# Optimization experiments

Measured on AMD Instinct MI355X. Metric: run time of the kernel, lower is better.

## Reference

```python
import jax, jax.numpy as jnp
import numpy as np

N_HEAD = 8
D = 512
D_K = D // N_HEAD  # 64
B, S = 8, 1024


def setup_inputs() -> dict:
    key = jax.random.key(0)
    ks = jax.random.split(key, 7)
    scale = 1.0 / np.sqrt(D)  # ~ torch Linear init range
    return {
        "q": jax.random.normal(ks[0], (B, S, D), dtype=jnp.float32),
        "k": jax.random.normal(ks[1], (B, S, D), dtype=jnp.float32),
        "v": jax.random.normal(ks[2], (B, S, D), dtype=jnp.float32),
        # per-head Q/K projection weights, torch Linear convention W:[out,in]=[d_k,d]
        "Wq": jax.random.uniform(ks[3], (N_HEAD, D_K, D), jnp.float32, -scale, scale),
        "Wk": jax.random.uniform(ks[4], (N_HEAD, D_K, D), jnp.float32, -scale, scale),
        "Wv": jax.random.uniform(ks[5], (D_K, D), jnp.float32, -scale, scale),
        "Wo": jax.random.uniform(ks[6], (D, D_K), jnpp := jnp.float32, -1.0 / np.sqrt(D_K), 1.0 / np.sqrt(D_K)),
    }


def reference(q, k, v, Wq, Wk, Wv, Wo):
    # shared V projection: [B,S,d_k]
    vs = jnp.einsum("bsd,ed->bse", v, Wv)
    # batched per-head Q/K projections: [B,H,S,d_k]
    qh = jnp.einsum("bsd,hed->bhse", q, Wq)
    kh = jnp.einsum("bsd,hed->bhse", k, Wk)
    inv_sqrt_dk = 1.0 / jnp.sqrt(jnp.asarray(D_K, q.dtype))
    # scores [B,H,Sq,Sk], softmax over keys
    scores = jnp.einsum("bhqe,bhke->bhqk", qh * inv_sqrt_dk, kh)
    attn = jax.nn.softmax(scores, axis=-1)
    # shared V across heads, then mean over heads (interpretable combine)
    heads = jnp.einsum("bhqk,bke->bhqe", attn, vs)  # [B,H,S,d_k]
    head = heads.mean(axis=1)                        # [B,S,d_k]
    out = jnp.einsum("bse,de->bsd", head, Wo)        # [B,S,d]
    # torch.stack(attention) stacks over heads first -> [H,B,Sq,Sk]
    attn_stacked = jnp.transpose(attn, (1, 0, 2, 3))
    return out, attn_stacked
```

## Files before the change

### kernel.cpp

```cpp
#include <hip/hip_runtime.h>


using short8 = __attribute__((ext_vector_type(8))) short;
using f32x4  = __attribute__((ext_vector_type(4))) float;

static __device__ __forceinline__ short f2bf(float f) {
    union { float f; unsigned u; } x; x.f = f;
    unsigned r = x.u + 0x7fffu + ((x.u >> 16) & 1u);
    return (short)(r >> 16);
}
static __device__ __forceinline__ float bfhi2f(unsigned hi_bits) {
    union { unsigned u; float f; } x; x.u = hi_bits;
    return x.f;
}

__global__ __launch_bounds__(256) void gemm_proj(
    const float* __restrict__ A, const float* __restrict__ W,
    void* __restrict__ out, int M, int N, int K, float scale, int mode)
{
    __shared__ short As[128][40];
    __shared__ short Bs[128][40];

    const int tid  = threadIdx.x;
    const int m0   = blockIdx.x * 128;
    const int n0   = blockIdx.y * 128;
    const int lane = tid & 63, wave = tid >> 6;
    const int wm   = (wave & 1) * 64, wn = (wave >> 1) * 64;
    const int lrow = lane & 15, lq = lane >> 4;

    f32x4 acc[4][4] = {};

    for (int k0 = 0; k0 < K; k0 += 32) {
#pragma unroll
        for (int i = 0; i < 4; ++i) {
            int c = tid + i * 256;
            int row = c >> 3, c4 = c & 7;
            float4 v = *(const float4*)(A + (size_t)(m0 + row) * K + k0 + c4 * 4);
            short* dst = &As[row][c4 * 4];
            dst[0] = f2bf(v.x); dst[1] = f2bf(v.y); dst[2] = f2bf(v.z); dst[3] = f2bf(v.w);
        }
#pragma unroll
        for (int i = 0; i < 4; ++i) {
            int c = tid + i * 256;
            int row = c >> 3, c4 = c & 7;
            int gn = n0 + row;
            float4 v = make_float4(0.f, 0.f, 0.f, 0.f);
            if (gn < N) v = *(const float4*)(W + (size_t)gn * K + k0 + c4 * 4);
            short* dst = &Bs[row][c4 * 4];
            dst[0] = f2bf(v.x); dst[1] = f2bf(v.y); dst[2] = f2bf(v.z); dst[3] = f2bf(v.w);
        }
        __syncthreads();

        short8 af[4], bw[4];
#pragma unroll
        for (int i = 0; i < 4; ++i)
            af[i] = *(const short8*)&As[wm + i * 16 + lrow][lq * 8];
#pragma unroll
        for (int j = 0; j < 4; ++j)
            bw[j] = *(const short8*)&Bs[wn + j * 16 + lrow][lq * 8];
#pragma unroll
        for (int i = 0; i < 4; ++i)
#pragma unroll
            for (int j = 0; j < 4; ++j)
                acc[i][j] = __builtin_amdgcn_mfma_f32_16x16x32_bf16(af[i], bw[j], acc[i][j], 0, 0, 0);
        __syncthreads();
    }

#pragma unroll
    for (int i = 0; i < 4; ++i) {
#pragma unroll
        for (int j = 0; j < 4; ++j) {
#pragma unroll
            for (int r = 0; r < 4; ++r) {
                int m = m0 + wm + i * 16 + lq * 4 + r;
                int n = n0 + wn + j * 16 + lrow;
                if (n >= N) continue;
                float val = acc[i][j][r] * scale;
                if (mode == 0) {
                    int b = m >> 10, s = m & 1023;
                    int hh = n >> 6, e = n & 63;
                    ((short*)out)[(((size_t)(b * 8 + hh) * 1024 + s) << 6) + e] = f2bf(val);
                } else if (mode == 2) {
                    int b = m >> 10, s = m & 1023;
                    ((short*)out)[(((size_t)b * 64 + n) << 10) + s] = f2bf(val);
                } else {
                    ((float*)out)[(size_t)m * N + n] = val;
                }
            }
        }
    }
}

__global__ __launch_bounds__(256) void attn_fused(
    const short* __restrict__ qh,
    const short* __restrict__ kh,
    const short* __restrict__ vt,
    float* __restrict__ attn_out,
    float* __restrict__ head)
{
    __shared__ short qs[64][72];
    __shared__ short ks[128][72];
    __shared__ short vts[64][136];
    __shared__ short pa[4][16][136];

    const int bh = blockIdx.x;
    const int b = bh >> 3, h = bh & 7;
    const int qbase = blockIdx.y << 6;
    const int tid  = threadIdx.x;
    const int lane = tid & 63, wave = tid >> 6;
    const int lrow = lane & 15, lq = lane >> 4;

    const short* qp = qh + ((size_t)bh << 16);
    const short* kp = kh + ((size_t)bh << 16);
    const short* vp = vt + ((size_t)b << 16);

#pragma unroll
    for (int i = 0; i < 2; ++i) {
        int c = tid + i * 256;
        int row = c >> 3, c8 = c & 7;
        *(uint4*)&qs[row][c8 * 8] = *(const uint4*)(qp + (size_t)(qbase + row) * 64 + c8 * 8);
    }
    __syncthreads();

    short8 qf[2];
#pragma unroll
    for (int kk = 0; kk < 2; ++kk)
        qf[kk] = *(const short8*)&qs[wave * 16 + lrow][kk * 32 + lq * 8];

    float sume[4] = {0.f, 0.f, 0.f, 0.f};
    for (int kt = 0; kt < 1024; kt += 128) {
        __syncthreads();
#pragma unroll
        for (int i = 0; i < 4; ++i) {
            int c = tid + i * 256;
            int row = c >> 3, c8 = c & 7;
            *(uint4*)&ks[row][c8 * 8] = *(const uint4*)(kp + (size_t)(kt + row) * 64 + c8 * 8);
        }
        __syncthreads();
#pragma unroll
        for (int j = 0; j < 8; ++j) {
            f32x4 sc = {0.f, 0.f, 0.f, 0.f};
            short8 kb0 = *(const short8*)&ks[j * 16 + lrow][lq * 8];
            short8 kb1 = *(const short8*)&ks[j * 16 + lrow][32 + lq * 8];
            sc = __builtin_amdgcn_mfma_f32_16x16x32_bf16(qf[0], kb0, sc, 0, 0, 0);
            sc = __builtin_amdgcn_mfma_f32_16x16x32_bf16(qf[1], kb1, sc, 0, 0, 0);
#pragma unroll
            for (int r = 0; r < 4; ++r) sume[r] += __expf(sc[r]);
        }
    }
#pragma unroll
    for (int m = 1; m <= 8; m <<= 1)
#pragma unroll
        for (int r = 0; r < 4; ++r) sume[r] += __shfl_xor(sume[r], m, 64);
    float rinv[4];
#pragma unroll
    for (int r = 0; r < 4; ++r) rinv[r] = 1.0f / sume[r];

    f32x4 hacc[4] = {};
    for (int kt = 0; kt < 1024; kt += 128) {
        __syncthreads();
#pragma unroll
        for (int i = 0; i < 4; ++i) {
            int c = tid + i * 256;
            int row = c >> 3, c8 = c & 7;
            *(uint4*)&ks[row][c8 * 8] = *(const uint4*)(kp + (size_t)(kt + row) * 64 + c8 * 8);
        }
#pragma unroll
        for (int i = 0; i < 4; ++i) {
            int c = tid + i * 256;
            int row = c >> 4, c8 = c & 15;
            *(uint4*)&vts[row][c8 * 8] = *(const uint4*)(vp + ((size_t)row << 10) + kt + c8 * 8);
        }
        __syncthreads();

#pragma unroll
        for (int j = 0; j < 8; ++j) {
            f32x4 sc = {0.f, 0.f, 0.f, 0.f};
            short8 kb0 = *(const short8*)&ks[j * 16 + lrow][lq * 8];
            short8 kb1 = *(const short8*)&ks[j * 16 + lrow][32 + lq * 8];
            sc = __builtin_amdgcn_mfma_f32_16x16x32_bf16(qf[0], kb0, sc, 0, 0, 0);
            sc = __builtin_amdgcn_mfma_f32_16x16x32_bf16(qf[1], kb1, sc, 0, 0, 0);
#pragma unroll
            for (int r = 0; r < 4; ++r)
                pa[wave][lq * 4 + r][j * 16 + lrow] = f2bf(__expf(sc[r]) * rinv[r]);
        }

        size_t abase = (((size_t)(h * 8 + b) * 1024 + qbase + wave * 16) << 10) + kt;
#pragma unroll
        for (int i = 0; i < 4; ++i) {
            int c = lane + i * 64;
            int row = c >> 4, c8 = c & 15;
            uint4 pk = *(const uint4*)&pa[wave][row][c8 * 8];
            float4 v0, v1;
            v0.x = bfhi2f(pk.x << 16); v0.y = bfhi2f(pk.x & 0xffff0000u);
            v0.z = bfhi2f(pk.y << 16); v0.w = bfhi2f(pk.y & 0xffff0000u);
            v1.x = bfhi2f(pk.z << 16); v1.y = bfhi2f(pk.z & 0xffff0000u);
            v1.z = bfhi2f(pk.w << 16); v1.w = bfhi2f(pk.w & 0xffff0000u);
            float* gdst = attn_out + abase + ((size_t)row << 10) + c8 * 8;
            *(float4*)gdst       = v0;
            *(float4*)(gdst + 4) = v1;
        }

#pragma unroll
        for (int kk = 0; kk < 4; ++kk) {
            short8 af = *(const short8*)&pa[wave][lrow][kk * 32 + lq * 8];
#pragma unroll
            for (int cc = 0; cc < 4; ++cc) {
                short8 bv = *(const short8*)&vts[cc * 16 + lrow][kk * 32 + lq * 8];
                hacc[cc] = __builtin_amdgcn_mfma_f32_16x16x32_bf16(af, bv, hacc[cc], 0, 0, 0);
            }
        }
    }

#pragma unroll
    for (int cc = 0; cc < 4; ++cc)
#pragma unroll
        for (int r = 0; r < 4; ++r) {
            float v = hacc[cc][r] * 0.125f;
            atomicAdd(&head[(((size_t)b * 1024 + qbase + wave * 16 + lq * 4 + r) << 6) + cc * 16 + lrow], v);
        }
}

extern "C" void kernel_launch(void* const* d_in, const int* in_sizes, int n_in,
                              void* d_out, int out_size, void* d_ws, size_t ws_size,
                              hipStream_t stream)
{
    (void)in_sizes; (void)n_in; (void)out_size; (void)ws_size;

    const float* q  = (const float*)d_in[0];
    const float* k  = (const float*)d_in[1];
    const float* v  = (const float*)d_in[2];
    const float* Wq = (const float*)d_in[3];
    const float* Wk = (const float*)d_in[4];
    const float* Wv = (const float*)d_in[5];
    const float* Wo = (const float*)d_in[6];

    float* out  = (float*)d_out;
    float* attn = out + (size_t)8 * 1024 * 512;

    char* ws = (char*)d_ws;
    short* qh  = (short*)(ws);
    short* kh  = (short*)(ws + ((size_t)8  << 20));
    short* vt  = (short*)(ws + ((size_t)16 << 20));
    float* head = (float*)(ws + ((size_t)17 << 20));

    hipMemsetAsync(head, 0, (size_t)8 * 1024 * 64 * sizeof(float), stream);

    gemm_proj<<<dim3(64, 4), 256, 0, stream>>>(q, Wq, qh, 8192, 512, 512, 0.125f, 0);
    gemm_proj<<<dim3(64, 4), 256, 0, stream>>>(k, Wk, kh, 8192, 512, 512, 1.0f, 0);
    gemm_proj<<<dim3(64, 1), 256, 0, stream>>>(v, Wv, vt, 8192, 64, 512, 1.0f, 2);

    attn_fused<<<dim3(64, 16), 256, 0, stream>>>(qh, kh, vt, attn, head);

    gemm_proj<<<dim3(64, 4), 256, 0, stream>>>(head, Wo, out, 8192, 512, 64, 1.0f, 3);
}
```

Before: 517.4 us.

## Merge projection launches, widen attention blocks, use nontemporal attn stores

The three Q/K/V projection GEMMs become one launch that picks its operands from blockIdx.y, and the output GEMM gets its own specialised kernel. The attention kernel now runs 512 threads covering 128 query rows per block, so each K/V tile loaded into LDS is shared by twice as many waves, halving K/V reloads. Attention probability stores use nontemporal writes to avoid polluting caches with the large write-once output. The larger blocks use more LDS and mean fewer blocks overall, which may lower occupancy.

```diff
diff --git a/kernel.cpp b/kernel.cpp
--- a/kernel.cpp
+++ b/kernel.cpp
@@ -14,16 +14,25 @@
     return x.f;
 }
 
-__global__ __launch_bounds__(256) void gemm_proj(
-    const float* __restrict__ A, const float* __restrict__ W,
-    void* __restrict__ out, int M, int N, int K, float scale, int mode)
+__global__ __launch_bounds__(256) void proj_all(
+    const float* __restrict__ q, const float* __restrict__ k,
+    const float* __restrict__ v,
+    const float* __restrict__ Wq, const float* __restrict__ Wk,
+    const float* __restrict__ Wv,
+    short* __restrict__ qh, short* __restrict__ kh, short* __restrict__ vt)
 {
     __shared__ short As[128][40];
     __shared__ short Bs[128][40];
 
+    const int y = blockIdx.y;
+    const float* A; const float* W; short* out; int N; float scale; int mode; int n0;
+    if (y < 4)      { A = q; W = Wq; out = qh; N = 512; scale = 0.125f; mode = 0; n0 = y << 7; }
+    else if (y < 8) { A = k; W = Wk; out = kh; N = 512; scale = 1.0f;   mode = 0; n0 = (y - 4) << 7; }
+    else            { A = v; W = Wv; out = vt; N = 64;  scale = 1.0f;   mode = 2; n0 = 0; }
+
+    const int K = 512;
     const int tid  = threadIdx.x;
     const int m0   = blockIdx.x * 128;
-    const int n0   = blockIdx.y * 128;
     const int lane = tid & 63, wave = tid >> 6;
     const int wm   = (wave & 1) * 64, wn = (wave >> 1) * 64;
     const int lrow = lane & 15, lq = lane >> 4;
@@ -35,19 +44,19 @@
         for (int i = 0; i < 4; ++i) {
             int c = tid + i * 256;
             int row = c >> 3, c4 = c & 7;
-            float4 v = *(const float4*)(A + (size_t)(m0 + row) * K + k0 + c4 * 4);
+            float4 vv = *(const float4*)(A + (size_t)(m0 + row) * K + k0 + c4 * 4);
             short* dst = &As[row][c4 * 4];
-            dst[0] = f2bf(v.x); dst[1] = f2bf(v.y); dst[2] = f2bf(v.z); dst[3] = f2bf(v.w);
+            dst[0] = f2bf(vv.x); dst[1] = f2bf(vv.y); dst[2] = f2bf(vv.z); dst[3] = f2bf(vv.w);
         }
 #pragma unroll
         for (int i = 0; i < 4; ++i) {
             int c = tid + i * 256;
             int row = c >> 3, c4 = c & 7;
             int gn = n0 + row;
-            float4 v = make_float4(0.f, 0.f, 0.f, 0.f);
-            if (gn < N) v = *(const float4*)(W + (size_t)gn * K + k0 + c4 * 4);
+            float4 vv = make_float4(0.f, 0.f, 0.f, 0.f);
+            if (gn < N) vv = *(const float4*)(W + (size_t)gn * K + k0 + c4 * 4);
             short* dst = &Bs[row][c4 * 4];
-            dst[0] = f2bf(v.x); dst[1] = f2bf(v.y); dst[2] = f2bf(v.z); dst[3] = f2bf(v.w);
+            dst[0] = f2bf(vv.x); dst[1] = f2bf(vv.y); dst[2] = f2bf(vv.z); dst[3] = f2bf(vv.w);
         }
         __syncthreads();
 
@@ -79,33 +88,96 @@
                 if (mode == 0) {
                     int b = m >> 10, s = m & 1023;
                     int hh = n >> 6, e = n & 63;
-                    ((short*)out)[(((size_t)(b * 8 + hh) * 1024 + s) << 6) + e] = f2bf(val);
-                } else if (mode == 2) {
+                    out[(((size_t)(b * 8 + hh) * 1024 + s) << 6) + e] = f2bf(val);
+                } else {
                     int b = m >> 10, s = m & 1023;
-                    ((short*)out)[(((size_t)b * 64 + n) << 10) + s] = f2bf(val);
-                } else {
-                    ((float*)out)[(size_t)m * N + n] = val;
+                    out[(((size_t)b * 64 + n) << 10) + s] = f2bf(val);
                 }
             }
         }
     }
 }
 
-__global__ __launch_bounds__(256) void attn_fused(
+__global__ __launch_bounds__(256) void gemm_out(
+    const float* __restrict__ A, const float* __restrict__ W,
+    float* __restrict__ out, int M, int N, int K)
+{
+    __shared__ short As[128][40];
+    __shared__ short Bs[128][40];
+
+    const int tid  = threadIdx.x;
+    const int m0   = blockIdx.x * 128;
+    const int n0   = blockIdx.y * 128;
+    const int lane = tid & 63, wave = tid >> 6;
+    const int wm   = (wave & 1) * 64, wn = (wave >> 1) * 64;
+    const int lrow = lane & 15, lq = lane >> 4;
+
+    f32x4 acc[4][4] = {};
+
+    for (int k0 = 0; k0 < K; k0 += 32) {
+#pragma unroll
+        for (int i = 0; i < 4; ++i) {
+            int c = tid + i * 256;
+            int row = c >> 3, c4 = c & 7;
+            float4 vv = *(const float4*)(A + (size_t)(m0 + row) * K + k0 + c4 * 4);
+            short* dst = &As[row][c4 * 4];
+            dst[0] = f2bf(vv.x); dst[1] = f2bf(vv.y); dst[2] = f2bf(vv.z); dst[3] = f2bf(vv.w);
+        }
+#pragma unroll
+        for (int i = 0; i < 4; ++i) {
+            int c = tid + i * 256;
+            int row = c >> 3, c4 = c & 7;
+            int gn = n0 + row;
+            float4 vv = make_float4(0.f, 0.f, 0.f, 0.f);
+            if (gn < N) vv = *(const float4*)(W + (size_t)gn * K + k0 + c4 * 4);
+            short* dst = &Bs[row][c4 * 4];
+            dst[0] = f2bf(vv.x); dst[1] = f2bf(vv.y); dst[2] = f2bf(vv.z); dst[3] = f2bf(vv.w);
+        }
+        __syncthreads();
+
+        short8 af[4], bw[4];
+#pragma unroll
+        for (int i = 0; i < 4; ++i)
+            af[i] = *(const short8*)&As[wm + i * 16 + lrow][lq * 8];
+#pragma unroll
+        for (int j = 0; j < 4; ++j)
+            bw[j] = *(const short8*)&Bs[wn + j * 16 + lrow][lq * 8];
+#pragma unroll
+        for (int i = 0; i < 4; ++i)
+#pragma unroll
+            for (int j = 0; j < 4; ++j)
+                acc[i][j] = __builtin_amdgcn_mfma_f32_16x16x32_bf16(af[i], bw[j], acc[i][j], 0, 0, 0);
+        __syncthreads();
+    }
+
+#pragma unroll
+    for (int i = 0; i < 4; ++i)
+#pragma unroll
+        for (int j = 0; j < 4; ++j)
+#pragma unroll
+            for (int r = 0; r < 4; ++r) {
+                int m = m0 + wm + i * 16 + lq * 4 + r;
+                int n = n0 + wn + j * 16 + lrow;
+                if (n >= N) continue;
+                out[(size_t)m * N + n] = acc[i][j][r];
+            }
+}
+
+__global__ __launch_bounds__(512) void attn_fused(
     const short* __restrict__ qh,
     const short* __restrict__ kh,
     const short* __restrict__ vt,
     float* __restrict__ attn_out,
     float* __restrict__ head)
 {
-    __shared__ short qs[64][72];
+    __shared__ short qs[128][72];
     __shared__ short ks[128][72];
     __shared__ short vts[64][136];
-    __shared__ short pa[4][16][136];
+    __shared__ short pa[8][16][136];
 
     const int bh = blockIdx.x;
     const int b = bh >> 3, h = bh & 7;
-    const int qbase = blockIdx.y << 6;
+    const int qbase = blockIdx.y << 7;
     const int tid  = threadIdx.x;
     const int lane = tid & 63, wave = tid >> 6;
     const int lrow = lane & 15, lq = lane >> 4;
@@ -116,7 +188,7 @@
 
 #pragma unroll
     for (int i = 0; i < 2; ++i) {
-        int c = tid + i * 256;
+        int c = tid + i * 512;
         int row = c >> 3, c8 = c & 7;
         *(uint4*)&qs[row][c8 * 8] = *(const uint4*)(qp + (size_t)(qbase + row) * 64 + c8 * 8);
     }
@@ -131,8 +203,8 @@
     for (int kt = 0; kt < 1024; kt += 128) {
         __syncthreads();
 #pragma unroll
-        for (int i = 0; i < 4; ++i) {
-            int c = tid + i * 256;
+        for (int i = 0; i < 2; ++i) {
+            int c = tid + i * 512;
             int row = c >> 3, c8 = c & 7;
             *(uint4*)&ks[row][c8 * 8] = *(const uint4*)(kp + (size_t)(kt + row) * 64 + c8 * 8);
         }
@@ -160,14 +232,14 @@
     for (int kt = 0; kt < 1024; kt += 128) {
         __syncthreads();
 #pragma unroll
-        for (int i = 0; i < 4; ++i) {
-            int c = tid + i * 256;
+        for (int i = 0; i < 2; ++i) {
+            int c = tid + i * 512;
             int row = c >> 3, c8 = c & 7;
             *(uint4*)&ks[row][c8 * 8] = *(const uint4*)(kp + (size_t)(kt + row) * 64 + c8 * 8);
         }
 #pragma unroll
-        for (int i = 0; i < 4; ++i) {
-            int c = tid + i * 256;
+        for (int i = 0; i < 2; ++i) {
+            int c = tid + i * 512;
             int row = c >> 4, c8 = c & 15;
             *(uint4*)&vts[row][c8 * 8] = *(const uint4*)(vp + ((size_t)row << 10) + kt + c8 * 8);
         }
@@ -191,14 +263,14 @@
             int c = lane + i * 64;
             int row = c >> 4, c8 = c & 15;
             uint4 pk = *(const uint4*)&pa[wave][row][c8 * 8];
-            float4 v0, v1;
+            f32x4 v0, v1;
             v0.x = bfhi2f(pk.x << 16); v0.y = bfhi2f(pk.x & 0xffff0000u);
             v0.z = bfhi2f(pk.y << 16); v0.w = bfhi2f(pk.y & 0xffff0000u);
             v1.x = bfhi2f(pk.z << 16); v1.y = bfhi2f(pk.z & 0xffff0000u);
             v1.z = bfhi2f(pk.w << 16); v1.w = bfhi2f(pk.w & 0xffff0000u);
             float* gdst = attn_out + abase + ((size_t)row << 10) + c8 * 8;
-            *(float4*)gdst       = v0;
-            *(float4*)(gdst + 4) = v1;
+            __builtin_nontemporal_store(v0, (f32x4*)gdst);
+            __builtin_nontemporal_store(v1, (f32x4*)(gdst + 4));
         }
 
 #pragma unroll
@@ -244,13 +316,11 @@
     short* vt  = (short*)(ws + ((size_t)16 << 20));
     float* head = (float*)(ws + ((size_t)17 << 20));
 
-    hipMemsetAsync(head, 0, (size_t)8 * 1024 * 64 * sizeof(float), stream);
-
-    gemm_proj<<<dim3(64, 4), 256, 0, stream>>>(q, Wq, qh, 8192, 512, 512, 0.125f, 0);
-    gemm_proj<<<dim3(64, 4), 256, 0, stream>>>(k, Wk, kh, 8192, 512, 512, 1.0f, 0);
-    gemm_proj<<<dim3(64, 1), 256, 0, stream>>>(v, Wv, vt, 8192, 64, 512, 1.0f, 2);
-
-    attn_fused<<<dim3(64, 16), 256, 0, stream>>>(qh, kh, vt, attn, head);
-
-    gemm_proj<<<dim3(64, 4), 256, 0, stream>>>(head, Wo, out, 8192, 512, 64, 1.0f, 3);
-}
+    (void)hipMemsetAsync(head, 0, (size_t)8 * 1024 * 64 * sizeof(float), stream);
+
+    proj_all<<<dim3(64, 9), 256, 0, stream>>>(q, k, v, Wq, Wk, Wv, qh, kh, vt);
+
+    attn_fused<<<dim3(64, 8), 512, 0, stream>>>(qh, kh, vt, attn, head);
+
+    gemm_out<<<dim3(64, 4), 256, 0, stream>>>(head, Wo, out, 8192, 512, 64);
+}
```

Result: faster. 455.1 us (-12.0%).
